# Optimization experiments

Hardware: AMD Instinct MI355X
Metric: run time of the kernel (lower is better)

Reference implementation:

```python
import jax, jax.numpy as jnp
import numpy as np

B, N, DEG = 16, 64, 16          # batch, nodes, out-degree per node
IN_F, EDGE_F, OUT_F, H = 1024, 128, 512, 8
F = OUT_F // H                   # n_hidden = 64 (is_concat=True)
E = N * DEG                      # num_edges = 1024
SLOPE = 0.2                      # leaky relu negative slope


def setup_inputs() -> dict:
    key = jax.random.key(0)
    k0, k1, k2, k3, k4 = jax.random.split(key, 5)
    h = jax.random.normal(k0, (B, N, IN_F), dtype=jnp.float32)
    edge_attr = jax.random.normal(k1, (B, E, EDGE_F), dtype=jnp.float32)
    # deterministic adjacency: node i -> nodes (i+k) % N, k=0..DEG-1
    # (includes self-loop, so every softmax row has >=1 neighbor)
    adj = np.zeros((N, N), dtype=np.float32)
    for i in range(N):
        for k in range(DEG):
            adj[i, (i + k) % N] = 1.0
    adj_mat = jnp.asarray(np.broadcast_to(adj, (B, N, N)).copy())
    W_node = jax.random.normal(k2, (IN_F, H * F), dtype=jnp.float32) * 0.03
    W_edge = jax.random.normal(k3, (EDGE_F, H * F), dtype=jnp.float32) * 0.05
    w_attn = jax.random.normal(k4, (3 * F,), dtype=jnp.float32) * 0.1
    return {"h": h, "adj_mat": adj_mat, "edge_attr": edge_attr,
            "W_node": W_node, "W_edge": W_edge, "w_attn": w_attn}


def reference(h, adj_mat, edge_attr, W_node, W_edge, w_attn):
    # node / edge projections
    g = (h @ W_node).reshape(B, N, H, F)                  # [B,N,H,F]
    e_proj = (edge_attr @ W_edge).reshape(B, E, H, F)     # [B,E,H,F]
    # pad edge rows up to N*N (mirrors torch.cat with zero pad)
    e_proj = jnp.pad(e_proj, ((0, 0), (0, N * N - E), (0, 0), (0, 0)))
    # scatter edge features to flattened nonzero adjacency positions,
    # in row-major nonzero order == rank via exclusive cumsum
    idx = adj_mat.reshape(B, N * N).astype(jnp.int32)     # [B,N*N] of 0/1
    rank = jnp.cumsum(idx, axis=1) - idx                  # position among nonzeros
    ef = jnp.take_along_axis(e_proj, rank[:, :, None, None], axis=1)
    ef = ef * idx[:, :, None, None].astype(g.dtype)       # zero where no edge
    ef = ef.reshape(B, N, N, H, F)                        # [B,i,j,H,F]
    # attn(cat[g_i, g_j, edge]) == g_i.w1 + g_j.w2 + edge.w3
    w_i, w_j, w_e = w_attn[:F], w_attn[F:2 * F], w_attn[2 * F:]
    s_i = jnp.einsum('bnhf,f->bnh', g, w_i)
    s_j = jnp.einsum('bnhf,f->bnh', g, w_j)
    s_e = jnp.einsum('bijhf,f->bijh', ef, w_e)
    e = jax.nn.leaky_relu(s_i[:, :, None, :] + s_j[:, None, :, :] + s_e, SLOPE)
    e = jnp.where(adj_mat[..., None] > 0, e, -jnp.inf)    # mask non-edges
    a = jax.nn.softmax(e, axis=2)                         # softmax over j
    # dropout is identity in eval mode
    out = jnp.einsum('bijh,bjhf->bihf', a, g)             # weighted aggregation
    return out.reshape(B, N, H * F)                       # is_concat=True
```

## Files before the change

kernel.cpp:

```cpp
#include <hip/hip_runtime.h>
#include <hip/hip_bf16.h>
#include <stdint.h>

#define SLOPE 0.2f

typedef short s16x8 __attribute__((ext_vector_type(8)));
typedef float f32x4 __attribute__((ext_vector_type(4)));

__device__ __forceinline__ unsigned short f2bf(float x) {
    union { float f; uint32_t u; } v; v.f = x;
    uint32_t u = v.u;
    return (unsigned short)((u + 0x7FFFu + ((u >> 16) & 1u)) >> 16);
}

__global__ __launch_bounds__(256)
void main_kernel(const float* __restrict__ hmat,
                 const float* __restrict__ adj,
                 const float* __restrict__ edge_attr,
                 const float* __restrict__ W_node,
                 const float* __restrict__ W_edge,
                 const float* __restrict__ w_attn,
                 float* __restrict__ g,
                 float* __restrict__ s_e,
                 float* __restrict__ s_i,
                 float* __restrict__ s_j,
                 int* __restrict__ row_start)
{
    __shared__ __align__(16) char U[20480];
    unsigned short* As = (unsigned short*)U;
    unsigned short* Bs = (unsigned short*)(U + 10240);
    float* wvs = (float*)U;

    int bx = blockIdx.x, tid = threadIdx.x;

    if (bx < 128) {
        int head = bx & 7, mt = bx >> 3;
        int n0 = head * 64, m0 = mt * 64;
        int wave = tid >> 6, lane = tid & 63;
        int l15 = lane & 15, quad = lane >> 4;
        int wv16 = wave * 16;

        int ldr = tid >> 2, ldc8 = (tid & 3) * 8;
        int kp = tid >> 4, nq = tid & 15;

        const float* apBase = hmat + (size_t)(m0 + ldr) * 1024 + ldc8;
        const float* bpBase = W_node + (size_t)(2 * kp) * 512 + n0 + nq * 4;

        f32x4 acc[4];
        #pragma unroll
        for (int i = 0; i < 4; ++i) acc[i] = (f32x4){0.f, 0.f, 0.f, 0.f};

        float4 a0 = *(const float4*)(apBase);
        float4 a1 = *(const float4*)(apBase + 4);
        float4 b0 = *(const float4*)(bpBase);
        float4 b1 = *(const float4*)(bpBase + 512);
        {
            s16x8 av;
            av[0] = (short)f2bf(a0.x); av[1] = (short)f2bf(a0.y);
            av[2] = (short)f2bf(a0.z); av[3] = (short)f2bf(a0.w);
            av[4] = (short)f2bf(a1.x); av[5] = (short)f2bf(a1.y);
            av[6] = (short)f2bf(a1.z); av[7] = (short)f2bf(a1.w);
            *(s16x8*)&As[ldr * 40 + ldc8] = av;
            const float* p0 = &b0.x; const float* p1 = &b1.x;
            #pragma unroll
            for (int u = 0; u < 4; ++u) {
                uint32_t pk = (uint32_t)f2bf(p0[u]) | ((uint32_t)f2bf(p1[u]) << 16);
                *(uint32_t*)&Bs[(nq * 4 + u) * 40 + 2 * kp] = pk;
            }
        }

        for (int it = 0; it < 32; ++it) {
            __syncthreads();
            if (it + 1 < 32) {
                const float* ap = apBase + (it + 1) * 32;
                a0 = *(const float4*)ap;
                a1 = *(const float4*)(ap + 4);
                const float* bp = bpBase + (size_t)(it + 1) * 32 * 512;
                b0 = *(const float4*)bp;
                b1 = *(const float4*)(bp + 512);
            }
            int cur = it & 1;
            s16x8 af = *(const s16x8*)&As[(cur * 64 + wv16 + l15) * 40 + quad * 8];
            #pragma unroll
            for (int nt = 0; nt < 4; ++nt) {
                s16x8 bf = *(const s16x8*)&Bs[(cur * 64 + nt * 16 + l15) * 40 + quad * 8];
                acc[nt] = __builtin_amdgcn_mfma_f32_16x16x32_bf16(af, bf, acc[nt], 0, 0, 0);
            }
            if (it + 1 < 32) {
                int nxt = cur ^ 1;
                s16x8 av;
                av[0] = (short)f2bf(a0.x); av[1] = (short)f2bf(a0.y);
                av[2] = (short)f2bf(a0.z); av[3] = (short)f2bf(a0.w);
                av[4] = (short)f2bf(a1.x); av[5] = (short)f2bf(a1.y);
                av[6] = (short)f2bf(a1.z); av[7] = (short)f2bf(a1.w);
                *(s16x8*)&As[(nxt * 64 + ldr) * 40 + ldc8] = av;
                const float* p0 = &b0.x; const float* p1 = &b1.x;
                #pragma unroll
                for (int u = 0; u < 4; ++u) {
                    uint32_t pk = (uint32_t)f2bf(p0[u]) | ((uint32_t)f2bf(p1[u]) << 16);
                    *(uint32_t*)&Bs[(nxt * 64 + nq * 4 + u) * 40 + 2 * kp] = pk;
                }
            }
        }

        float wi[4], wj[4];
        #pragma unroll
        for (int nt = 0; nt < 4; ++nt) {
            wi[nt] = w_attn[nt * 16 + l15];
            wj[nt] = w_attn[64 + nt * 16 + l15];
        }
        float pi[4], pj[4];
        #pragma unroll
        for (int reg = 0; reg < 4; ++reg) { pi[reg] = 0.f; pj[reg] = 0.f; }
        #pragma unroll
        for (int nt = 0; nt < 4; ++nt) {
            #pragma unroll
            for (int reg = 0; reg < 4; ++reg) {
                int gm = m0 + wv16 + quad * 4 + reg;
                int gn = n0 + nt * 16 + l15;
                g[(size_t)gm * 512 + gn] = acc[nt][reg];
                pi[reg] += acc[nt][reg] * wi[nt];
                pj[reg] += acc[nt][reg] * wj[nt];
            }
        }
        #pragma unroll
        for (int mask = 1; mask < 16; mask <<= 1) {
            #pragma unroll
            for (int reg = 0; reg < 4; ++reg) {
                pi[reg] += __shfl_xor(pi[reg], mask);
                pj[reg] += __shfl_xor(pj[reg], mask);
            }
        }
        if (l15 == 0) {
            #pragma unroll
            for (int reg = 0; reg < 4; ++reg) {
                int r = m0 + wv16 + quad * 4 + reg;
                s_i[(size_t)r * 8 + head] = pi[reg];
                s_j[(size_t)r * 8 + head] = pj[reg];
            }
        }
    } else if (bx < 192) {
        {
            int c = tid & 127, half = tid >> 7;
            const float* we = w_attn + 128;
            #pragma unroll
            for (int hh = 0; hh < 4; ++hh) {
                int h = half * 4 + hh;
                float s = 0.f;
                const float* row = W_edge + (size_t)c * 512 + h * 64;
                #pragma unroll 8
                for (int f = 0; f < 64; ++f) s += row[f] * we[f];
                wvs[c * 8 + h] = s;
            }
        }
        __syncthreads();
        int e = (bx - 128) * 256 + tid;
        const float4* erow = (const float4*)(edge_attr + (size_t)e * 128);
        f32x4 accl = {0.f, 0.f, 0.f, 0.f};
        f32x4 acch = {0.f, 0.f, 0.f, 0.f};
        for (int c4 = 0; c4 < 32; ++c4) {
            float4 v = erow[c4];
            #pragma unroll
            for (int u = 0; u < 4; ++u) {
                int c = c4 * 4 + u;
                f32x4 w0 = *(const f32x4*)&wvs[c * 8];
                f32x4 w1 = *(const f32x4*)&wvs[c * 8 + 4];
                float x = (u == 0) ? v.x : (u == 1) ? v.y : (u == 2) ? v.z : v.w;
                accl += x * w0;
                acch += x * w1;
            }
        }
        *(f32x4*)(s_e + (size_t)e * 8)     = accl;
        *(f32x4*)(s_e + (size_t)e * 8 + 4) = acch;
    } else {
        int b = bx - 192;
        if (tid < 64) {
            const float* row = adj + (size_t)b * 4096 + (size_t)tid * 64;
            int cnt = 0;
            #pragma unroll 8
            for (int j = 0; j < 64; ++j) cnt += (row[j] > 0.5f) ? 1 : 0;
            int inc = cnt;
            #pragma unroll
            for (int d = 1; d < 64; d <<= 1) {
                int u = __shfl_up(inc, d, 64);
                if (tid >= d) inc += u;
            }
            row_start[b * 64 + tid] = inc - cnt;
        }
    }
}

__global__ __launch_bounds__(256)
void attn_kernel(const float* __restrict__ g,
                 const float* __restrict__ adj,
                 const float* __restrict__ s_e,
                 const float* __restrict__ s_i,
                 const float* __restrict__ s_j,
                 const int*   __restrict__ row_start,
                 float* __restrict__ out)
{
    __shared__ __align__(16) float gs[16][516];
    __shared__ float se_s[16][8];
    __shared__ float sj_s[16][8];
    __shared__ float a_s[16][8];
    __shared__ float si_s[8];
    __shared__ int nbr[16];
    __shared__ int m_nb_s;

    int bi = blockIdx.x;
    int b = bi >> 6, i = bi & 63;
    int tid = threadIdx.x;

    if (tid < 64) {
        float av = adj[(size_t)b * 4096 + (size_t)i * 64 + tid];
        unsigned long long m = __ballot(av > 0.5f);
        if (av > 0.5f) {
            int before = __popcll(m & ((1ull << tid) - 1ull));
            if (before < 16) nbr[before] = tid;
        }
        if (tid == 0) {
            int c = __popcll(m);
            m_nb_s = (c > 16) ? 16 : c;
        }
    }
    __syncthreads();

    int m_nb = m_nb_s;
    int rs = row_start[bi];

    int slot = tid >> 4, l16 = tid & 15;
    if (slot < m_nb) {
        const float4* src4 = (const float4*)(g + (size_t)(b * 64 + nbr[slot]) * 512);
        #pragma unroll
        for (int j = 0; j < 8; ++j) {
            int q = j * 16 + l16;
            *(float4*)&gs[slot][q * 4] = src4[q];
        }
    }
    if (tid < 128) {
        int k = tid >> 3, h = tid & 7;
        if (k < m_nb) {
            se_s[k][h] = s_e[(size_t)(b * 1024 + rs + k) * 8 + h];
            sj_s[k][h] = s_j[(size_t)(b * 64 + nbr[k]) * 8 + h];
        }
    } else if (tid < 136) {
        si_s[tid - 128] = s_i[(size_t)bi * 8 + (tid - 128)];
    }
    __syncthreads();

    if (tid < 8) {
        int h = tid;
        float si = si_s[h];
        float sc[16];
        float mx = -1e30f;
        for (int k = 0; k < m_nb; ++k) {
            float v = si + sj_s[k][h] + se_s[k][h];
            v = (v >= 0.f) ? v : SLOPE * v;
            sc[k] = v;
            mx = fmaxf(mx, v);
        }
        float ssum = 0.f;
        for (int k = 0; k < m_nb; ++k) {
            float e = __expf(sc[k] - mx);
            a_s[k][h] = e;
            ssum += e;
        }
        float inv = 1.f / ssum;
        for (int k = 0; k < m_nb; ++k) a_s[k][h] *= inv;
    }
    __syncthreads();

    int c0 = tid * 2;
    int h = tid >> 5;
    float a0 = 0.f, a1 = 0.f;
    for (int k = 0; k < m_nb; ++k) {
        float ak = a_s[k][h];
        a0 += ak * gs[k][c0];
        a1 += ak * gs[k][c0 + 1];
    }
    out[(size_t)bi * 512 + c0]     = a0;
    out[(size_t)bi * 512 + c0 + 1] = a1;
}

extern "C" void kernel_launch(void* const* d_in, const int* in_sizes, int n_in,
                              void* d_out, int out_size, void* d_ws, size_t ws_size,
                              hipStream_t stream) {
    const float* h_in      = (const float*)d_in[0];
    const float* adj_mat   = (const float*)d_in[1];
    const float* edge_attr = (const float*)d_in[2];
    const float* W_node    = (const float*)d_in[3];
    const float* W_edge    = (const float*)d_in[4];
    const float* w_attn    = (const float*)d_in[5];
    float* out = (float*)d_out;

    char* ws = (char*)d_ws;
    float* g         = (float*)(ws + 0x000000);
    float* s_e       = (float*)(ws + 0x200000);
    float* s_i       = (float*)(ws + 0x280000);
    float* s_j       = (float*)(ws + 0x288000);
    int*   row_start = (int*)  (ws + 0x290000);

    main_kernel<<<208, 256, 0, stream>>>(h_in, adj_mat, edge_attr,
                                         W_node, W_edge, w_attn,
                                         g, s_e, s_i, s_j, row_start);
    attn_kernel<<<1024, 256, 0, stream>>>(g, adj_mat, s_e, s_i, s_j,
                                          row_start, out);
}
```

Baseline: 97.47 us.

## Load GEMM A fragments directly into registers and restructure attention softmax with shuffles

In the projection GEMM, each lane now loads its own A-operand fragment from global memory and converts it to bf16 in registers, removing the A shared-memory tile and its stores. The scalar bf16 rounding is replaced by the packed v_cvt_pk_bf16_f32 instruction. The attention kernel drops its shared staging of g and score arrays: each thread reads its neighbour g values straight into registers, and the per-head softmax runs across 16 lanes with xor-shuffle reductions instead of 8 serial threads. This cuts LDS traffic and barriers, at the cost of less coalesced A loads, more registers, and always reading 16 neighbours (unused slots point at node 0).

```diff
diff --git a/kernel.cpp b/kernel.cpp
--- a/kernel.cpp
+++ b/kernel.cpp
@@ -7,10 +7,10 @@
 typedef short s16x8 __attribute__((ext_vector_type(8)));
 typedef float f32x4 __attribute__((ext_vector_type(4)));
 
-__device__ __forceinline__ unsigned short f2bf(float x) {
-    union { float f; uint32_t u; } v; v.f = x;
-    uint32_t u = v.u;
-    return (unsigned short)((u + 0x7FFFu + ((u >> 16) & 1u)) >> 16);
+__device__ __forceinline__ uint32_t pk_bf16(float lo, float hi) {
+    uint32_t r;
+    asm("v_cvt_pk_bf16_f32 %0, %1, %2" : "=v"(r) : "v"(lo), "v"(hi));
+    return r;
 }
 
 __global__ __launch_bounds__(256)
@@ -26,9 +26,8 @@
                  float* __restrict__ s_j,
                  int* __restrict__ row_start)
 {
-    __shared__ __align__(16) char U[20480];
-    unsigned short* As = (unsigned short*)U;
-    unsigned short* Bs = (unsigned short*)(U + 10240);
+    __shared__ __align__(16) char U[10240];
+    unsigned short* Bs = (unsigned short*)U;
     float* wvs = (float*)U;
 
     int bx = blockIdx.x, tid = threadIdx.x;
@@ -40,39 +39,37 @@
         int l15 = lane & 15, quad = lane >> 4;
         int wv16 = wave * 16;
 
-        int ldr = tid >> 2, ldc8 = (tid & 3) * 8;
         int kp = tid >> 4, nq = tid & 15;
 
-        const float* apBase = hmat + (size_t)(m0 + ldr) * 1024 + ldc8;
+        const float* aFrag  = hmat + (size_t)(m0 + wv16 + l15) * 1024 + quad * 8;
         const float* bpBase = W_node + (size_t)(2 * kp) * 512 + n0 + nq * 4;
 
         f32x4 acc[4];
         #pragma unroll
         for (int i = 0; i < 4; ++i) acc[i] = (f32x4){0.f, 0.f, 0.f, 0.f};
 
-        float4 a0 = *(const float4*)(apBase);
-        float4 a1 = *(const float4*)(apBase + 4);
+        float4 a0 = *(const float4*)(aFrag);
+        float4 a1 = *(const float4*)(aFrag + 4);
         float4 b0 = *(const float4*)(bpBase);
         float4 b1 = *(const float4*)(bpBase + 512);
         {
-            s16x8 av;
-            av[0] = (short)f2bf(a0.x); av[1] = (short)f2bf(a0.y);
-            av[2] = (short)f2bf(a0.z); av[3] = (short)f2bf(a0.w);
-            av[4] = (short)f2bf(a1.x); av[5] = (short)f2bf(a1.y);
-            av[6] = (short)f2bf(a1.z); av[7] = (short)f2bf(a1.w);
-            *(s16x8*)&As[ldr * 40 + ldc8] = av;
-            const float* p0 = &b0.x; const float* p1 = &b1.x;
-            #pragma unroll
-            for (int u = 0; u < 4; ++u) {
-                uint32_t pk = (uint32_t)f2bf(p0[u]) | ((uint32_t)f2bf(p1[u]) << 16);
-                *(uint32_t*)&Bs[(nq * 4 + u) * 40 + 2 * kp] = pk;
-            }
+            *(uint32_t*)&Bs[(nq * 4 + 0) * 40 + 2 * kp] = pk_bf16(b0.x, b1.x);
+            *(uint32_t*)&Bs[(nq * 4 + 1) * 40 + 2 * kp] = pk_bf16(b0.y, b1.y);
+            *(uint32_t*)&Bs[(nq * 4 + 2) * 40 + 2 * kp] = pk_bf16(b0.z, b1.z);
+            *(uint32_t*)&Bs[(nq * 4 + 3) * 40 + 2 * kp] = pk_bf16(b0.w, b1.w);
         }
 
         for (int it = 0; it < 32; ++it) {
+            union { s16x8 v; uint32_t w[4]; } A;
+            A.w[0] = pk_bf16(a0.x, a0.y);
+            A.w[1] = pk_bf16(a0.z, a0.w);
+            A.w[2] = pk_bf16(a1.x, a1.y);
+            A.w[3] = pk_bf16(a1.z, a1.w);
+
             __syncthreads();
+
             if (it + 1 < 32) {
-                const float* ap = apBase + (it + 1) * 32;
+                const float* ap = aFrag + (it + 1) * 32;
                 a0 = *(const float4*)ap;
                 a1 = *(const float4*)(ap + 4);
                 const float* bp = bpBase + (size_t)(it + 1) * 32 * 512;
@@ -80,7 +77,7 @@
                 b1 = *(const float4*)(bp + 512);
             }
             int cur = it & 1;
-            s16x8 af = *(const s16x8*)&As[(cur * 64 + wv16 + l15) * 40 + quad * 8];
+            s16x8 af = A.v;
             #pragma unroll
             for (int nt = 0; nt < 4; ++nt) {
                 s16x8 bf = *(const s16x8*)&Bs[(cur * 64 + nt * 16 + l15) * 40 + quad * 8];
@@ -88,18 +85,10 @@
             }
             if (it + 1 < 32) {
                 int nxt = cur ^ 1;
-                s16x8 av;
-                av[0] = (short)f2bf(a0.x); av[1] = (short)f2bf(a0.y);
-                av[2] = (short)f2bf(a0.z); av[3] = (short)f2bf(a0.w);
-                av[4] = (short)f2bf(a1.x); av[5] = (short)f2bf(a1.y);
-                av[6] = (short)f2bf(a1.z); av[7] = (short)f2bf(a1.w);
-                *(s16x8*)&As[(nxt * 64 + ldr) * 40 + ldc8] = av;
-                const float* p0 = &b0.x; const float* p1 = &b1.x;
-                #pragma unroll
-                for (int u = 0; u < 4; ++u) {
-                    uint32_t pk = (uint32_t)f2bf(p0[u]) | ((uint32_t)f2bf(p1[u]) << 16);
-                    *(uint32_t*)&Bs[(nxt * 64 + nq * 4 + u) * 40 + 2 * kp] = pk;
-                }
+                *(uint32_t*)&Bs[(nxt * 64 + nq * 4 + 0) * 40 + 2 * kp] = pk_bf16(b0.x, b1.x);
+                *(uint32_t*)&Bs[(nxt * 64 + nq * 4 + 1) * 40 + 2 * kp] = pk_bf16(b0.y, b1.y);
+                *(uint32_t*)&Bs[(nxt * 64 + nq * 4 + 2) * 40 + 2 * kp] = pk_bf16(b0.z, b1.z);
+                *(uint32_t*)&Bs[(nxt * 64 + nq * 4 + 3) * 40 + 2 * kp] = pk_bf16(b0.w, b1.w);
             }
         }
 
@@ -199,11 +188,7 @@
                  const int*   __restrict__ row_start,
                  float* __restrict__ out)
 {
-    __shared__ __align__(16) float gs[16][516];
-    __shared__ float se_s[16][8];
-    __shared__ float sj_s[16][8];
     __shared__ float a_s[16][8];
-    __shared__ float si_s[8];
     __shared__ int nbr[16];
     __shared__ int m_nb_s;
 
@@ -211,6 +196,7 @@
     int b = bi >> 6, i = bi & 63;
     int tid = threadIdx.x;
 
+    if (tid < 16) nbr[tid] = 0;
     if (tid < 64) {
         float av = adj[(size_t)b * 4096 + (size_t)i * 64 + tid];
         unsigned long long m = __ballot(av > 0.5f);
@@ -226,60 +212,50 @@
     __syncthreads();
 
     int m_nb = m_nb_s;
-    int rs = row_start[bi];
-
-    int slot = tid >> 4, l16 = tid & 15;
-    if (slot < m_nb) {
-        const float4* src4 = (const float4*)(g + (size_t)(b * 64 + nbr[slot]) * 512);
-        #pragma unroll
-        for (int j = 0; j < 8; ++j) {
-            int q = j * 16 + l16;
-            *(float4*)&gs[slot][q * 4] = src4[q];
-        }
-    }
-    if (tid < 128) {
-        int k = tid >> 3, h = tid & 7;
-        if (k < m_nb) {
-            se_s[k][h] = s_e[(size_t)(b * 1024 + rs + k) * 8 + h];
-            sj_s[k][h] = s_j[(size_t)(b * 64 + nbr[k]) * 8 + h];
-        }
-    } else if (tid < 136) {
-        si_s[tid - 128] = s_i[(size_t)bi * 8 + (tid - 128)];
-    }
-    __syncthreads();
-
-    if (tid < 8) {
-        int h = tid;
-        float si = si_s[h];
-        float sc[16];
-        float mx = -1e30f;
-        for (int k = 0; k < m_nb; ++k) {
-            float v = si + sj_s[k][h] + se_s[k][h];
-            v = (v >= 0.f) ? v : SLOPE * v;
-            sc[k] = v;
-            mx = fmaxf(mx, v);
-        }
-        float ssum = 0.f;
-        for (int k = 0; k < m_nb; ++k) {
-            float e = __expf(sc[k] - mx);
-            a_s[k][h] = e;
-            ssum += e;
-        }
-        float inv = 1.f / ssum;
-        for (int k = 0; k < m_nb; ++k) a_s[k][h] *= inv;
-    }
-    __syncthreads();
 
     int c0 = tid * 2;
     int h = tid >> 5;
-    float a0 = 0.f, a1 = 0.f;
-    for (int k = 0; k < m_nb; ++k) {
+    float2 gv[16];
+    #pragma unroll
+    for (int k = 0; k < 16; ++k) {
+        gv[k] = *(const float2*)(g + (size_t)(b * 64 + nbr[k]) * 512 + c0);
+    }
+
+    if (tid < 128) {
+        int hh = tid >> 4, k = tid & 15;
+        float v;
+        if (k < m_nb) {
+            int rs = row_start[bi];
+            float se = s_e[(size_t)(b * 1024 + rs + k) * 8 + hh];
+            float sj = s_j[(size_t)(b * 64 + nbr[k]) * 8 + hh];
+            float si = s_i[(size_t)bi * 8 + hh];
+            v = si + sj + se;
+            v = (v >= 0.f) ? v : SLOPE * v;
+        } else {
+            v = -1e30f;
+        }
+        float mx = v;
+        #pragma unroll
+        for (int mask = 1; mask < 16; mask <<= 1)
+            mx = fmaxf(mx, __shfl_xor(mx, mask));
+        float e = (k < m_nb) ? __expf(v - mx) : 0.f;
+        float ssum = e;
+        #pragma unroll
+        for (int mask = 1; mask < 16; mask <<= 1)
+            ssum += __shfl_xor(ssum, mask);
+        a_s[k][hh] = e / ssum;
+    }
+    __syncthreads();
+
+    float o0 = 0.f, o1 = 0.f;
+    #pragma unroll
+    for (int k = 0; k < 16; ++k) {
         float ak = a_s[k][h];
-        a0 += ak * gs[k][c0];
-        a1 += ak * gs[k][c0 + 1];
-    }
-    out[(size_t)bi * 512 + c0]     = a0;
-    out[(size_t)bi * 512 + c0 + 1] = a1;
+        o0 += ak * gv[k].x;
+        o1 += ak * gv[k].y;
+    }
+    out[(size_t)bi * 512 + c0]     = o0;
+    out[(size_t)bi * 512 + c0 + 1] = o1;
 }
 
 extern "C" void kernel_launch(void* const* d_in, const int* in_sizes, int n_in,
```

New measurement: 91.43 us. 6.2% less time.
